# Kernel optimization log

Hardware: AMD Instinct MI355X
Metric: run time of the kernel (lower is better)

Reference implementation:

```python
import jax, jax.numpy as jnp
import numpy as np

OUT_FEATURES = 11008
IN_FEATURES = 4096
GROUP_SIZE = 32
N_GROUPS = OUT_FEATURES * IN_FEATURES // GROUP_SIZE  # 1409024
LEVELS = jnp.array([-1.0, -0.333, 0.333, 1.0], dtype=jnp.float32)


def setup_inputs() -> dict:
    key = jax.random.key(0)
    k1, k2, k3, k4 = jax.random.split(key, 4)
    x = jax.random.normal(k1, (16, IN_FEATURES), dtype=jnp.float32)
    weight_q2 = jax.random.randint(k2, (N_GROUPS, GROUP_SIZE // 4), 0, 256, dtype=jnp.int32)
    weight_norm = jax.random.uniform(k3, (N_GROUPS, 1), dtype=jnp.float32).astype(jnp.float16)
    bias = jax.random.normal(k4, (OUT_FEATURES,), dtype=jnp.float32)
    return {"x": x, "weight_q2": weight_q2, "weight_norm": weight_norm, "bias": bias}


def _dequantize_2bit(packed, norm):
    # packed: [G, group/4] int; element at group-column 4*k+i comes from bits [2i:2i+2) of packed[:, k]
    shifts = jnp.array([0, 2, 4, 6], dtype=jnp.int32)
    codes = (packed[:, :, None] >> shifts[None, None, :]) & 3  # [G, group/4, 4]
    x_q = LEVELS[codes].reshape(packed.shape[0], -1)  # [G, group]
    return x_q * norm.astype(jnp.float32)  # per-group scale


def reference(x, weight_q2, weight_norm, bias):
    weight = _dequantize_2bit(weight_q2, weight_norm).reshape(OUT_FEATURES, IN_FEATURES).astype(x.dtype)
    return x @ weight.T + bias.astype(x.dtype)
```

## Files before the change

### kernel.cpp

```cpp
#include <hip/hip_runtime.h>
#include <hip/hip_fp16.h>

#define OUTF 11008
#define INF  4096
#define NTILES 688

typedef unsigned int uint;
typedef __attribute__((ext_vector_type(8))) _Float16 f16x8;
typedef __attribute__((ext_vector_type(4))) float f32x4;

typedef __attribute__((address_space(1))) void gvoid_t;
typedef __attribute__((address_space(3))) void svoid_t;

union UA { uint4 u4; uint u[4]; f16x8 v; };
union UH { uint u; __half2 h; };
union USH { unsigned short s; __half h; };

#define WAITV(n) asm volatile("s_waitcnt vmcnt(" #n ")" ::: "memory")
#define FENCE()  asm volatile("" ::: "memory")
#define BARRIER() { FENCE(); __builtin_amdgcn_s_barrier(); FENCE(); }

__global__ __launch_bounds__(256, 3) void lin2bit_kernel(
    const float* __restrict__ x, const int* __restrict__ wq,
    const float* __restrict__ wn, const float* __restrict__ bias,
    float* __restrict__ out)
{
  __shared__ __align__(16) char lds[51200];
  char* LUT = lds;
  char* NL  = lds + 2048;
  char* X0  = lds + 10240;
  char* X1  = lds + 26624;
  char* W0  = lds + 43008;
  char* W1  = lds + 47104;

  const int tid = threadIdx.x;
  const int wv  = tid >> 6;
  const int l   = tid & 63;
  const int col = l & 15;
  const int q   = l >> 4;
  const int o0  = (int)blockIdx.x << 4;

  const char* xb  = (const char*)x;
  const char* wqb = (const char*)wq;
  const char* wnb = (const char*)wn;

  {
#pragma unroll
    for (int ii = 0; ii < 2; ++ii) {
      const int i = wv * 2 + ii;
      const int r = 2 * i + (l >> 5);
      const char* src = wnb + (size_t)(o0 + r) * 512 + (((l & 31) ^ (r & 7)) << 4);
      __builtin_amdgcn_global_load_lds((gvoid_t*)src,
                                       (svoid_t*)(NL + i * 1024 + l * 16), 16, 0, 0);
    }
  }
  FENCE();

#define STAGE_X(c, buf) { \
    _Pragma("unroll") \
    for (int ii = 0; ii < 4; ++ii) { \
      const int i = wv * 4 + ii; \
      const char* src = xb + (size_t)i * 16384 + (size_t)(c) * 1024 \
                        + ((((l >> 1) ^ (i & 7)) << 5) | ((l & 1) << 4)); \
      __builtin_amdgcn_global_load_lds((gvoid_t*)src, \
                                       (svoid_t*)((buf) + i * 1024 + l * 16), 16, 0, 0); \
    } }

#define STAGE_W(c, buf) { \
    const int r = wv * 4 + (l >> 4); \
    const char* src = wqb + (size_t)(o0 + r) * 4096 + (size_t)(c) * 256 \
                      + (((l & 15) ^ (r & 7)) << 4); \
    __builtin_amdgcn_global_load_lds((gvoid_t*)src, \
                                     (svoid_t*)((buf) + wv * 1024 + l * 16), 16, 0, 0); }

  STAGE_X(0, X0); STAGE_W(0, W0); FENCE();
  STAGE_X(1, X1); STAGE_W(1, W1); FENCE();

  {
    USH h0, h1, h2, h3;
    h0.h = __float2half(-1.0f);  h1.h = __float2half(-0.333f);
    h2.h = __float2half(0.333f); h3.h = __float2half(1.0f);
    const uint hv[4] = {h0.s, h1.s, h2.s, h3.s};
#pragma unroll
    for (int e = 0; e < 4; ++e) {
      const int idx = e * 64 + l;
      const uint lo = hv[idx & 3]        | (hv[(idx >> 2) & 3] << 16);
      const uint hi = hv[(idx >> 4) & 3] | (hv[(idx >> 6) & 3] << 16);
      *(uint2*)(LUT + idx * 8) = make_uint2(lo, hi);
    }
  }

  f32x4 acc = {0.f, 0.f, 0.f, 0.f};
  const int c7 = col & 7;

#define COMPUTE(c, xs, ws) { \
    const int naddr = col * 512 + ((((c) * 2 + (wv >> 1)) ^ c7) << 4) + (wv & 1) * 8; \
    const float2 nn = *(const float2*)(NL + naddr); \
    _Pragma("unroll") \
    for (int jj = 0; jj < 2; ++jj) { \
      const int g = wv * 2 + jj; \
      const float nv = jj ? nn.y : nn.x; \
      UH nvh; nvh.h = __floats2half2_rn(nv, nv); \
      const uint2 p = *(const uint2*)((ws) + col * 256 \
                        + (((g * 2 + (q >> 1)) ^ c7) << 4) + (q & 1) * 8); \
      const int xaddr = col * 1024 + (((g * 4 + q) ^ c7) << 5); \
      const float4 xa = *(const float4*)((xs) + xaddr); \
      const float4 xc = *(const float4*)((xs) + xaddr + 16); \
      UH k0, k1, k2, k3; \
      k0.h = __floats2half2_rn(xa.x, xa.y); k1.h = __floats2half2_rn(xa.z, xa.w); \
      k2.h = __floats2half2_rn(xc.x, xc.y); k3.h = __floats2half2_rn(xc.z, xc.w); \
      UA A; A.u[0] = k0.u; A.u[1] = k1.u; A.u[2] = k2.u; A.u[3] = k3.u; \
      const uint2 e0 = *(const uint2*)(LUT + ((size_t)(uint)p.x << 3)); \
      const uint2 e1 = *(const uint2*)(LUT + ((size_t)(uint)p.y << 3)); \
      UH a0, a1, a2, a3, b0, b1, b2, b3; \
      a0.u = e0.x; a1.u = e0.y; a2.u = e1.x; a3.u = e1.y; \
      b0.h = __hmul2(a0.h, nvh.h); b1.h = __hmul2(a1.h, nvh.h); \
      b2.h = __hmul2(a2.h, nvh.h); b3.h = __hmul2(a3.h, nvh.h); \
      UA B; B.u[0] = b0.u; B.u[1] = b1.u; B.u[2] = b2.u; B.u[3] = b3.u; \
      acc = __builtin_amdgcn_mfma_f32_16x16x32_f16(A.v, B.v, acc, 0, 0, 0); \
    } }

#define ITER_FULL(c, XS, WS) \
  WAITV(5); BARRIER(); \
  COMPUTE(c, XS, WS) \
  BARRIER(); \
  STAGE_X((c) + 2, XS); STAGE_W((c) + 2, WS); FENCE();

  ITER_FULL(0,  X0, W0)  ITER_FULL(1,  X1, W1)
  ITER_FULL(2,  X0, W0)  ITER_FULL(3,  X1, W1)
  ITER_FULL(4,  X0, W0)  ITER_FULL(5,  X1, W1)
  ITER_FULL(6,  X0, W0)  ITER_FULL(7,  X1, W1)
  ITER_FULL(8,  X0, W0)  ITER_FULL(9,  X1, W1)
  ITER_FULL(10, X0, W0)  ITER_FULL(11, X1, W1)
  ITER_FULL(12, X0, W0)  ITER_FULL(13, X1, W1)
  WAITV(5); BARRIER(); COMPUTE(14, X0, W0)
  WAITV(0); BARRIER(); COMPUTE(15, X1, W1)
#undef ITER_FULL
#undef COMPUTE
#undef STAGE_X
#undef STAGE_W

  __syncthreads();
  float* red = (float*)lds;
  red[wv * 256 +   0 + l] = acc[0];
  red[wv * 256 +  64 + l] = acc[1];
  red[wv * 256 + 128 + l] = acc[2];
  red[wv * 256 + 192 + l] = acc[3];
  __syncthreads();
  const int t = tid;
  const float s = red[t] + red[256 + t] + red[512 + t] + red[768 + t];
  const int m  = ((t & 63) >> 4) * 4 + (t >> 6);
  const int oc = t & 15;
  out[(size_t)m * OUTF + o0 + oc] = s + bias[o0 + oc];
}

extern "C" void kernel_launch(void* const* d_in, const int* in_sizes, int n_in,
                              void* d_out, int out_size, void* d_ws, size_t ws_size,
                              hipStream_t stream) {
  (void)in_sizes; (void)n_in; (void)out_size; (void)d_ws; (void)ws_size;
  const float* x    = (const float*)d_in[0];
  const int*   wq   = (const int*)d_in[1];
  const float* wn   = (const float*)d_in[2];
  const float* bias = (const float*)d_in[3];
  float*       out  = (float*)d_out;
  lin2bit_kernel<<<dim3(NTILES), dim3(256), 0, stream>>>(x, wq, wn, bias, out);
}
```

Baseline: 19.66 us.

## Double output rows per block to share staged activation tiles across two halves

Each block now computes 32 output features with 512 threads instead of 16 features with 256 threads. Waves are split into four K-slices and two output halves. The 16-row activation tile staged in LDS is shared by both halves, which halves activation staging per output row. Norm and weight staging, the vmcnt waits and the final cross-wave reduction are adjusted to match. The cost is more LDS per block and half as many blocks, which changes occupancy and tail balance across CUs.

```diff
diff --git a/kernel.cpp b/kernel.cpp
--- a/kernel.cpp
+++ b/kernel.cpp
@@ -3,7 +3,7 @@
 
 #define OUTF 11008
 #define INF  4096
-#define NTILES 688
+#define NBLK 344
 
 typedef unsigned int uint;
 typedef __attribute__((ext_vector_type(8))) _Float16 f16x8;
@@ -20,25 +20,27 @@
 #define FENCE()  asm volatile("" ::: "memory")
 #define BARRIER() { FENCE(); __builtin_amdgcn_s_barrier(); FENCE(); }
 
-__global__ __launch_bounds__(256, 3) void lin2bit_kernel(
+__global__ __launch_bounds__(512, 4) void lin2bit_kernel(
     const float* __restrict__ x, const int* __restrict__ wq,
     const float* __restrict__ wn, const float* __restrict__ bias,
     float* __restrict__ out)
 {
-  __shared__ __align__(16) char lds[51200];
+  __shared__ __align__(16) char lds[67584];
   char* LUT = lds;
   char* NL  = lds + 2048;
-  char* X0  = lds + 10240;
-  char* X1  = lds + 26624;
-  char* W0  = lds + 43008;
-  char* W1  = lds + 47104;
+  char* X0  = lds + 18432;
+  char* X1  = lds + 34816;
+  char* W0  = lds + 51200;
+  char* W1  = lds + 59392;
 
   const int tid = threadIdx.x;
   const int wv  = tid >> 6;
+  const int kq  = wv >> 1;
+  const int oh  = wv & 1;
   const int l   = tid & 63;
   const int col = l & 15;
   const int q   = l >> 4;
-  const int o0  = (int)blockIdx.x << 4;
+  const int o0  = (int)blockIdx.x << 5;
 
   const char* xb  = (const char*)x;
   const char* wqb = (const char*)wq;
@@ -58,12 +60,12 @@
 
 #define STAGE_X(c, buf) { \
     _Pragma("unroll") \
-    for (int ii = 0; ii < 4; ++ii) { \
-      const int i = wv * 4 + ii; \
-      const char* src = xb + (size_t)i * 16384 + (size_t)(c) * 1024 \
-                        + ((((l >> 1) ^ (i & 7)) << 5) | ((l & 1) << 4)); \
+    for (int jj = 0; jj < 2; ++jj) { \
+      const int j = wv * 2 + jj; \
+      const char* src = xb + (size_t)j * 16384 + (size_t)(c) * 1024 \
+                        + ((((l >> 1) ^ (j & 7)) << 5) | ((l & 1) << 4)); \
       __builtin_amdgcn_global_load_lds((gvoid_t*)src, \
-                                       (svoid_t*)((buf) + i * 1024 + l * 16), 16, 0, 0); \
+                                       (svoid_t*)((buf) + j * 1024 + l * 16), 16, 0, 0); \
     } }
 
 #define STAGE_W(c, buf) { \
@@ -91,19 +93,20 @@
   }
 
   f32x4 acc = {0.f, 0.f, 0.f, 0.f};
-  const int c7 = col & 7;
+  const int c7  = col & 7;
+  const int ol  = oh * 16 + col;
 
 #define COMPUTE(c, xs, ws) { \
-    const int naddr = col * 512 + ((((c) * 2 + (wv >> 1)) ^ c7) << 4) + (wv & 1) * 8; \
-    const float2 nn = *(const float2*)(NL + naddr); \
+    const float2 nn = *(const float2*)(NL + ol * 512 \
+                        + ((((c) * 2 + (kq >> 1)) ^ c7) << 4) + (kq & 1) * 8); \
     _Pragma("unroll") \
     for (int jj = 0; jj < 2; ++jj) { \
-      const int g = wv * 2 + jj; \
+      const int lg = kq * 2 + jj; \
       const float nv = jj ? nn.y : nn.x; \
       UH nvh; nvh.h = __floats2half2_rn(nv, nv); \
-      const uint2 p = *(const uint2*)((ws) + col * 256 \
-                        + (((g * 2 + (q >> 1)) ^ c7) << 4) + (q & 1) * 8); \
-      const int xaddr = col * 1024 + (((g * 4 + q) ^ c7) << 5); \
+      const uint2 p = *(const uint2*)((ws) + ol * 256 \
+                        + (((lg * 2 + (q >> 1)) ^ c7) << 4) + (q & 1) * 8); \
+      const int xaddr = col * 1024 + (((lg * 4 + q) ^ c7) << 5); \
       const float4 xa = *(const float4*)((xs) + xaddr); \
       const float4 xc = *(const float4*)((xs) + xaddr + 16); \
       UH k0, k1, k2, k3; \
@@ -121,7 +124,7 @@
     } }
 
 #define ITER_FULL(c, XS, WS) \
-  WAITV(5); BARRIER(); \
+  WAITV(3); BARRIER(); \
   COMPUTE(c, XS, WS) \
   BARRIER(); \
   STAGE_X((c) + 2, XS); STAGE_W((c) + 2, WS); FENCE();
@@ -133,7 +136,7 @@
   ITER_FULL(8,  X0, W0)  ITER_FULL(9,  X1, W1)
   ITER_FULL(10, X0, W0)  ITER_FULL(11, X1, W1)
   ITER_FULL(12, X0, W0)  ITER_FULL(13, X1, W1)
-  WAITV(5); BARRIER(); COMPUTE(14, X0, W0)
+  WAITV(3); BARRIER(); COMPUTE(14, X0, W0)
   WAITV(0); BARRIER(); COMPUTE(15, X1, W1)
 #undef ITER_FULL
 #undef COMPUTE
@@ -148,10 +151,14 @@
   red[wv * 256 + 192 + l] = acc[3];
   __syncthreads();
   const int t = tid;
-  const float s = red[t] + red[256 + t] + red[512 + t] + red[768 + t];
-  const int m  = ((t & 63) >> 4) * 4 + (t >> 6);
-  const int oc = t & 15;
-  out[(size_t)m * OUTF + o0 + oc] = s + bias[o0 + oc];
+  const int oh2 = t >> 8;
+  const int r2  = t & 255;
+  float s = red[(0 * 2 + oh2) * 256 + r2] + red[(1 * 2 + oh2) * 256 + r2]
+          + red[(2 * 2 + oh2) * 256 + r2] + red[(3 * 2 + oh2) * 256 + r2];
+  const int i2 = r2 >> 6, l2 = r2 & 63;
+  const int m  = ((l2 >> 4) << 2) + i2;
+  const int oc = o0 + oh2 * 16 + (l2 & 15);
+  out[(size_t)m * OUTF + oc] = s + bias[oc];
 }
 
 extern "C" void kernel_launch(void* const* d_in, const int* in_sizes, int n_in,
@@ -163,5 +170,5 @@
   const float* wn   = (const float*)d_in[2];
   const float* bias = (const float*)d_in[3];
   float*       out  = (float*)d_out;
-  lin2bit_kernel<<<dim3(NTILES), dim3(256), 0, stream>>>(x, wq, wn, bias, out);
+  lin2bit_kernel<<<dim3(NBLK), dim3(512), 0, stream>>>(x, wq, wn, bias, out);
 }
```

Result: slower. 20.31 us (+3.3%).

## Stage x through registers as fp16 in LDS to halve X buffers and raise occupancy

Applied to the files above, without the earlier changes.

Activations are now loaded into registers with global_load_dwordx4, converted to fp16 once, and written to LDS, instead of being copied as fp32 straight into LDS and converted inside every compute step. This halves the X staging buffers, shrinking LDS from 51200 to 34816 bytes so launch bounds can ask for 4 blocks per CU instead of 3. The compute step reads one packed uint4 of fp16 A operand instead of two float4 loads plus conversions. The price is a register round trip, manual vmcnt/lgkmcnt waits and an extra barrier per iteration, which may add latency to the pipeline.

```diff
diff --git a/kernel.cpp b/kernel.cpp
--- a/kernel.cpp
+++ b/kernel.cpp
@@ -17,21 +17,23 @@
 union USH { unsigned short s; __half h; };
 
 #define WAITV(n) asm volatile("s_waitcnt vmcnt(" #n ")" ::: "memory")
+#define WAITL()  asm volatile("s_waitcnt lgkmcnt(0)" ::: "memory")
+#define SBAR()   __builtin_amdgcn_sched_barrier(0)
 #define FENCE()  asm volatile("" ::: "memory")
 #define BARRIER() { FENCE(); __builtin_amdgcn_s_barrier(); FENCE(); }
 
-__global__ __launch_bounds__(256, 3) void lin2bit_kernel(
+__global__ __launch_bounds__(256, 4) void lin2bit_kernel(
     const float* __restrict__ x, const int* __restrict__ wq,
     const float* __restrict__ wn, const float* __restrict__ bias,
     float* __restrict__ out)
 {
-  __shared__ __align__(16) char lds[51200];
+  __shared__ __align__(16) char lds[34816];
   char* LUT = lds;
   char* NL  = lds + 2048;
   char* X0  = lds + 10240;
-  char* X1  = lds + 26624;
-  char* W0  = lds + 43008;
-  char* W1  = lds + 47104;
+  char* X1  = lds + 18432;
+  char* W0  = lds + 26624;
+  char* W1  = lds + 30720;
 
   const int tid = threadIdx.x;
   const int wv  = tid >> 6;
@@ -56,25 +58,38 @@
   }
   FENCE();
 
-#define STAGE_X(c, buf) { \
+#define XLOAD(c, xr) { \
     _Pragma("unroll") \
-    for (int ii = 0; ii < 4; ++ii) { \
-      const int i = wv * 4 + ii; \
-      const char* src = xb + (size_t)i * 16384 + (size_t)(c) * 1024 \
-                        + ((((l >> 1) ^ (i & 7)) << 5) | ((l & 1) << 4)); \
-      __builtin_amdgcn_global_load_lds((gvoid_t*)src, \
-                                       (svoid_t*)((buf) + i * 1024 + l * 16), 16, 0, 0); \
+    for (int rr = 0; rr < 4; ++rr) { \
+      const int r = wv * 4 + rr; \
+      const float* srcp = (const float*)(xb + (size_t)r * 16384 + (size_t)(c) * 1024) + l * 4; \
+      asm volatile("global_load_dwordx4 %0, %1, off" \
+                   : "=&v"((xr)[rr]) : "v"(srcp) : "memory"); \
     } }
 
-#define STAGE_W(c, buf) { \
+#define XWRITE(buf, xr) { \
+    _Pragma("unroll") \
+    for (int rr = 0; rr < 4; ++rr) { \
+      const int r = wv * 4 + rr; \
+      UH h0, h1; \
+      h0.h = __floats2half2_rn((xr)[rr].x, (xr)[rr].y); \
+      h1.h = __floats2half2_rn((xr)[rr].z, (xr)[rr].w); \
+      *(uint2*)((buf) + r * 512 + (((l >> 1) ^ (r & 7)) << 4) + (l & 1) * 8) = \
+          make_uint2(h0.u, h1.u); \
+    } }
+
+#define WSTAGE(c, buf) { \
     const int r = wv * 4 + (l >> 4); \
     const char* src = wqb + (size_t)(o0 + r) * 4096 + (size_t)(c) * 256 \
                       + (((l & 15) ^ (r & 7)) << 4); \
     __builtin_amdgcn_global_load_lds((gvoid_t*)src, \
                                      (svoid_t*)((buf) + wv * 1024 + l * 16), 16, 0, 0); }
 
-  STAGE_X(0, X0); STAGE_W(0, W0); FENCE();
-  STAGE_X(1, X1); STAGE_W(1, W1); FENCE();
+  float4 xrA[4], xrB[4];
+  XLOAD(0, xrA);   FENCE();
+  WSTAGE(0, W0);   FENCE();
+  XLOAD(1, xrB);   FENCE();
+  WSTAGE(1, W1);   FENCE();
 
   {
     USH h0, h1, h2, h3;
@@ -90,12 +105,16 @@
     }
   }
 
+  WAITV(5); SBAR();
+  XWRITE(X0, xrA);
+  WAITL(); BARRIER();
+
   f32x4 acc = {0.f, 0.f, 0.f, 0.f};
   const int c7 = col & 7;
 
 #define COMPUTE(c, xs, ws) { \
-    const int naddr = col * 512 + ((((c) * 2 + (wv >> 1)) ^ c7) << 4) + (wv & 1) * 8; \
-    const float2 nn = *(const float2*)(NL + naddr); \
+    const float2 nn = *(const float2*)(NL + col * 512 \
+                        + ((((c) * 2 + (wv >> 1)) ^ c7) << 4) + (wv & 1) * 8); \
     _Pragma("unroll") \
     for (int jj = 0; jj < 2; ++jj) { \
       const int g = wv * 2 + jj; \
@@ -103,13 +122,7 @@
       UH nvh; nvh.h = __floats2half2_rn(nv, nv); \
       const uint2 p = *(const uint2*)((ws) + col * 256 \
                         + (((g * 2 + (q >> 1)) ^ c7) << 4) + (q & 1) * 8); \
-      const int xaddr = col * 1024 + (((g * 4 + q) ^ c7) << 5); \
-      const float4 xa = *(const float4*)((xs) + xaddr); \
-      const float4 xc = *(const float4*)((xs) + xaddr + 16); \
-      UH k0, k1, k2, k3; \
-      k0.h = __floats2half2_rn(xa.x, xa.y); k1.h = __floats2half2_rn(xa.z, xa.w); \
-      k2.h = __floats2half2_rn(xc.x, xc.y); k3.h = __floats2half2_rn(xc.z, xc.w); \
-      UA A; A.u[0] = k0.u; A.u[1] = k1.u; A.u[2] = k2.u; A.u[3] = k3.u; \
+      UA A; A.u4 = *(const uint4*)((xs) + col * 512 + (((g * 4 + q) ^ c7) << 4)); \
       const uint2 e0 = *(const uint2*)(LUT + ((size_t)(uint)p.x << 3)); \
       const uint2 e1 = *(const uint2*)(LUT + ((size_t)(uint)p.y << 3)); \
       UH a0, a1, a2, a3, b0, b1, b2, b3; \
@@ -120,25 +133,40 @@
       acc = __builtin_amdgcn_mfma_f32_16x16x32_f16(A.v, B.v, acc, 0, 0, 0); \
     } }
 
-#define ITER_FULL(c, XS, WS) \
-  WAITV(5); BARRIER(); \
-  COMPUTE(c, XS, WS) \
+#define ITER_FULL(c, XC, WC, XN, XRC, XRN) \
+  COMPUTE(c, XC, WC) \
+  XLOAD((c) + 2, XRC);  FENCE(); \
   BARRIER(); \
-  STAGE_X((c) + 2, XS); STAGE_W((c) + 2, WS); FENCE();
+  WSTAGE((c) + 2, WC);  FENCE(); \
+  WAITV(5); SBAR(); \
+  XWRITE(XN, XRN); \
+  WAITL(); BARRIER();
 
-  ITER_FULL(0,  X0, W0)  ITER_FULL(1,  X1, W1)
-  ITER_FULL(2,  X0, W0)  ITER_FULL(3,  X1, W1)
-  ITER_FULL(4,  X0, W0)  ITER_FULL(5,  X1, W1)
-  ITER_FULL(6,  X0, W0)  ITER_FULL(7,  X1, W1)
-  ITER_FULL(8,  X0, W0)  ITER_FULL(9,  X1, W1)
-  ITER_FULL(10, X0, W0)  ITER_FULL(11, X1, W1)
-  ITER_FULL(12, X0, W0)  ITER_FULL(13, X1, W1)
-  WAITV(5); BARRIER(); COMPUTE(14, X0, W0)
-  WAITV(0); BARRIER(); COMPUTE(15, X1, W1)
+  ITER_FULL(0,  X0, W0, X1, xrA, xrB)
+  ITER_FULL(1,  X1, W1, X0, xrB, xrA)
+  ITER_FULL(2,  X0, W0, X1, xrA, xrB)
+  ITER_FULL(3,  X1, W1, X0, xrB, xrA)
+  ITER_FULL(4,  X0, W0, X1, xrA, xrB)
+  ITER_FULL(5,  X1, W1, X0, xrB, xrA)
+  ITER_FULL(6,  X0, W0, X1, xrA, xrB)
+  ITER_FULL(7,  X1, W1, X0, xrB, xrA)
+  ITER_FULL(8,  X0, W0, X1, xrA, xrB)
+  ITER_FULL(9,  X1, W1, X0, xrB, xrA)
+  ITER_FULL(10, X0, W0, X1, xrA, xrB)
+  ITER_FULL(11, X1, W1, X0, xrB, xrA)
+  ITER_FULL(12, X0, W0, X1, xrA, xrB)
+  ITER_FULL(13, X1, W1, X0, xrB, xrA)
+  COMPUTE(14, X0, W0)
+  BARRIER();
+  WAITV(0); SBAR();
+  XWRITE(X1, xrB);
+  WAITL(); BARRIER();
+  COMPUTE(15, X1, W1)
 #undef ITER_FULL
 #undef COMPUTE
-#undef STAGE_X
-#undef STAGE_W
+#undef XLOAD
+#undef XWRITE
+#undef WSTAGE
 
   __syncthreads();
   float* red = (float*)lds;
```

New measurement: 19.66 us. Within noise of the previous version (+0.0%).
